# Kernel optimization log

Measured on AMD Instinct MI355X. Metric: run time of the kernel, lower is better.

## Reference

```python
import jax, jax.numpy as jnp
import numpy as np


def _sage_conv(x, src, dst, W_l, b_l, W_r, num_nodes):
    # PyG SAGEConv (aggr='mean'): out = lin_l(mean_j x[src_j]) + lin_r(x)
    msg = x[src]                                                  # [E, d]
    agg = jax.ops.segment_sum(msg, dst, num_segments=num_nodes)   # [N, d]
    deg = jax.ops.segment_sum(jnp.ones_like(dst, dtype=x.dtype), dst,
                              num_segments=num_nodes)             # [N]
    mean = agg / jnp.maximum(deg, 1.0)[:, None]
    return mean @ W_l + b_l + x @ W_r


def setup_inputs() -> dict:
    key = jax.random.key(0)
    ks = jax.random.split(key, 8)
    N, E, D = 50000, 640000, 128
    s = 1.0 / np.sqrt(D)
    return {
        "x": jax.random.normal(ks[0], (N, D), dtype=jnp.float32),
        "edge_index": jax.random.randint(ks[1], (2, E), 0, N, dtype=jnp.int64),
        "W1_l": jax.random.normal(ks[2], (D, D), dtype=jnp.float32) * s,
        "b1_l": jnp.zeros((D,), dtype=jnp.float32),
        "W1_r": jax.random.normal(ks[3], (D, D), dtype=jnp.float32) * s,
        "W2_l": jax.random.normal(ks[4], (D, D), dtype=jnp.float32) * s,
        "b2_l": jnp.zeros((D,), dtype=jnp.float32),
        "W2_r": jax.random.normal(ks[5], (D, D), dtype=jnp.float32) * s,
    }


def reference(x, edge_index, W1_l, b1_l, W1_r, W2_l, b2_l, W2_r):
    N = x.shape[0]
    src, dst = edge_index[0], edge_index[1]
    h = jax.nn.relu(_sage_conv(x, src, dst, W1_l, b1_l, W1_r, N))
    z = _sage_conv(h, src, dst, W2_l, b2_l, W2_r, N)
    return z
```

## Files before the change

### kernel.cpp

```cpp
#include <hip/hip_runtime.h>
#include <hip/hip_bf16.h>


#define CAP 64
#define NBLKA 128

#if __has_builtin(__builtin_amdgcn_global_load_lds)
#define HAS_GLDS 1
#endif

typedef __attribute__((ext_vector_type(8))) short short8v;
typedef __attribute__((ext_vector_type(4))) float float4v;

__device__ __forceinline__ ushort f2bf(float f) {
    unsigned u = __float_as_uint(f);
    u += 0x7fff + ((u >> 16) & 1);
    return (ushort)(u >> 16);
}

#if __has_builtin(__builtin_amdgcn_cvt_pk_fp8_f32) && __has_builtin(__builtin_amdgcn_cvt_f32_fp8)
#define HW_FP8 1
#endif

__device__ __forceinline__ float fp8_dec_sw(unsigned b) {
    unsigned s = b >> 7, e = (b >> 3) & 15, m = b & 7;
    float v = e ? __uint_as_float(((e + 120u) << 23) | (m << 20))
                : (float)m * 0.001953125f;
    return s ? -v : v;
}
__device__ __forceinline__ unsigned fp8_enc_sw(float f) {
    float aa = fabsf(f);
    unsigned e32 = __float_as_uint(aa) >> 23;
    float c = (aa < 0.015625f) ? 16384.f : __uint_as_float((e32 + 20) << 23);
    float r = (aa + c) - c;
    if (r > 448.f) r = 448.f;
    unsigned s = (__float_as_uint(f) >> 31) << 7;
    if (r == 0.f) return s;
    unsigned u = __float_as_uint(r);
    int e = (int)(u >> 23) - 127;
    if (e < -6) return s | (unsigned)(r * 512.f);
    return s | ((unsigned)(e + 7) << 3) | ((u >> 20) & 7);
}

__device__ __forceinline__ unsigned enc4_fp8(float4 v) {
#ifdef HW_FP8
    int p = 0;
    p = __builtin_amdgcn_cvt_pk_fp8_f32(v.x, v.y, p, false);
    p = __builtin_amdgcn_cvt_pk_fp8_f32(v.z, v.w, p, true);
    return (unsigned)p;
#else
    return fp8_enc_sw(v.x) | (fp8_enc_sw(v.y) << 8) |
           (fp8_enc_sw(v.z) << 16) | (fp8_enc_sw(v.w) << 24);
#endif
}
__device__ __forceinline__ unsigned char enc1_fp8(float v) {
#ifdef HW_FP8
    return (unsigned char)(__builtin_amdgcn_cvt_pk_fp8_f32(v, v, 0, false) & 0xff);
#else
    return (unsigned char)fp8_enc_sw(v);
#endif
}
template <int SEL>
__device__ __forceinline__ float dec_fp8(unsigned w) {
#ifdef HW_FP8
    return __builtin_amdgcn_cvt_f32_fp8(w, SEL);
#else
    return fp8_dec_sw((w >> (SEL * 8)) & 0xff);
#endif
}
__device__ __forceinline__ void acc4_fp8(float* a, unsigned w) {
    a[0] += dec_fp8<0>(w);
    a[1] += dec_fp8<1>(w);
    a[2] += dec_fp8<2>(w);
    a[3] += dec_fp8<3>(w);
}

__global__ __launch_bounds__(256) void prep_bin_kernel(
    const int* __restrict__ src, const int* __restrict__ dst, int E, int N, int nbuk,
    unsigned* __restrict__ seg, int* __restrict__ cntA,
    const float* __restrict__ X, ushort* __restrict__ Xb,
    unsigned* __restrict__ X8, int n4,
    const float* __restrict__ W1l, const float* __restrict__ W1r, ushort* __restrict__ Wt1,
    const float* __restrict__ W2l, const float* __restrict__ W2r, ushort* __restrict__ Wt2,
    int nConv) {
    int b = blockIdx.x;
    if (b < NBLKA) {
        __shared__ int cnt[512];
        for (int i = threadIdx.x; i < nbuk; i += 256) cnt[i] = 0;
        __syncthreads();
        const int EPB = ((E + NBLKA - 1) / NBLKA + 3) & ~3;
        const int e0 = b * EPB;
        const int e1 = min(E & ~3, e0 + EPB);
        const int4* d4p = reinterpret_cast<const int4*>(dst);
        const int4* s4p = reinterpret_cast<const int4*>(src);
        unsigned* myseg = seg + (size_t)b * nbuk * CAP;
        for (int e4 = (e0 >> 2) + threadIdx.x; e4 < (e1 >> 2); e4 += 256) {
            int4 d4 = d4p[e4];
            int4 s4 = s4p[e4];
#pragma unroll
            for (int j = 0; j < 4; ++j) {
                int d = (&d4.x)[j];
                int bu = d >> 8;
                int pos = atomicAdd(&cnt[bu], 1);
                if (pos < CAP)
                    myseg[bu * CAP + pos] =
                        ((unsigned)(d & 255) << 16) | (unsigned)((&s4.x)[j] & 0xffff);
            }
        }
        if (b == 0) {
            int t = threadIdx.x;
            if (t < (E & 3)) {
                int e = (E & ~3) + t;
                int d = dst[e];
                int bu = d >> 8;
                int pos = atomicAdd(&cnt[bu], 1);
                if (pos < CAP)
                    myseg[bu * CAP + pos] =
                        ((unsigned)(d & 255) << 16) | (unsigned)(src[e] & 0xffff);
            }
        }
        __syncthreads();
        for (int i = threadIdx.x; i < nbuk; i += 256)
            cntA[b * nbuk + i] = min(cnt[i], CAP);
    } else if (b < NBLKA + nConv) {
        int i = (b - NBLKA) * 256 + threadIdx.x;
        if (i < n4) {
            float4 v = reinterpret_cast<const float4*>(X)[i];
            ushort4 o;
            o.x = f2bf(v.x); o.y = f2bf(v.y); o.z = f2bf(v.z); o.w = f2bf(v.w);
            reinterpret_cast<ushort4*>(Xb)[i] = o;
            X8[i] = enc4_fp8(v);
        }
    } else {
        int wb = b - NBLKA - nConv;
        const float* Wl = (wb < 128) ? W1l : W2l;
        const float* Wr = (wb < 128) ? W1r : W2r;
        ushort* Wt = (wb < 128) ? Wt1 : Wt2;
        int col = wb & 127;
        int k = threadIdx.x;
        float v = (k < 128) ? Wl[k * 128 + col] : Wr[(k - 128) * 128 + col];
        int gr = k >> 3, sub = k & 7;
        Wt[(size_t)(col * 32 + (gr ^ (col & 7))) * 8 + sub] = f2bf(v);
    }
}

__global__ __launch_bounds__(256) void csr_build_kernel(
    const unsigned* __restrict__ seg, const int* __restrict__ cntA,
    ushort* __restrict__ csrc, int* __restrict__ cursor, int N, int nbuk) {
    __shared__ ushort lcs[256 * CAP];
    __shared__ int lcnt[256];
    __shared__ int scnt[NBLKA];
    const int b = blockIdx.x;
    const int tid = threadIdx.x;
    lcnt[tid] = 0;
    if (tid < NBLKA) scnt[tid] = cntA[tid * nbuk + b];
    __syncthreads();
    for (int idx = tid; idx < NBLKA * CAP; idx += 256) {
        int blk = idx >> 6, slot = idx & (CAP - 1);
        if (slot < scnt[blk]) {
            unsigned en = seg[((size_t)blk * nbuk + b) * CAP + slot];
            int local = (en >> 16) & 255;
            int pos = atomicAdd(&lcnt[local], 1);
            if (pos < CAP) lcs[local * CAP + pos] = (ushort)(en & 0xffff);
        }
    }
    __syncthreads();
    const int maxNode = min(256, N - b * 256);
    const uint4* s4 = reinterpret_cast<const uint4*>(lcs);
    uint4* d4 = reinterpret_cast<uint4*>(csrc + (size_t)b * 256 * CAP);
    for (int i = tid; i < maxNode * (CAP / 8); i += 256) d4[i] = s4[i];
    if (tid < maxNode) cursor[b * 256 + tid] = min(lcnt[tid], CAP);
}

__global__ __launch_bounds__(256) void gather_mean_fp8(
    const unsigned* __restrict__ X8, const int* __restrict__ cnt,
    const ushort* __restrict__ csrc, ushort* __restrict__ meanb, int N) {
    const int wid = __builtin_amdgcn_readfirstlane((blockIdx.x * 256 + threadIdx.x) >> 6);
    if (wid >= N) return;
    const int lane = threadIdx.x & 63;
    const int q = lane >> 4;
    const int lq = lane & 15;
    const int dc = min(cnt[wid], CAP);
    const ushort* ep = csrc + (size_t)wid * CAP;

    float acc[8];
#pragma unroll
    for (int j = 0; j < 8; ++j) acc[j] = 0.f;

    const uint2* Xp = reinterpret_cast<const uint2*>(X8);
    int e = 0;
#pragma unroll 4
    for (; e + 3 < dc; e += 4) {
        uint2 iw = *reinterpret_cast<const uint2*>(ep + e);
        unsigned wv = (q & 2) ? iw.y : iw.x;
        int s = (q & 1) ? (int)(wv >> 16) : (int)(wv & 0xffff);
        uint2 v = Xp[(size_t)s * 16 + lq];
        acc4_fp8(acc, v.x);
        acc4_fp8(acc + 4, v.y);
    }
    if (e + q < dc) {
        int s = ep[e + q];
        uint2 v = Xp[(size_t)s * 16 + lq];
        acc4_fp8(acc, v.x);
        acc4_fp8(acc + 4, v.y);
    }

#pragma unroll
    for (int j = 0; j < 8; ++j) {
        acc[j] += __shfl_xor(acc[j], 32);
        acc[j] += __shfl_xor(acc[j], 16);
    }

    if (q == 0) {
        float sc = 1.0f / (float)max(dc, 1);
        uint4 o;
        o.x = (unsigned)f2bf(acc[0] * sc) | ((unsigned)f2bf(acc[1] * sc) << 16);
        o.y = (unsigned)f2bf(acc[2] * sc) | ((unsigned)f2bf(acc[3] * sc) << 16);
        o.z = (unsigned)f2bf(acc[4] * sc) | ((unsigned)f2bf(acc[5] * sc) << 16);
        o.w = (unsigned)f2bf(acc[6] * sc) | ((unsigned)f2bf(acc[7] * sc) << 16);
        reinterpret_cast<uint4*>(meanb)[(size_t)wid * 16 + lq] = o;
    }
}

template <int RELU, int OUT_BF16, int WRITE_FP8>
__global__ __launch_bounds__(256) void sage_gemm_mfma(
    const ushort* __restrict__ A0,
    const ushort* __restrict__ A1,
    const ushort* __restrict__ Wt,
    const float* __restrict__ bias,
    void* __restrict__ outv,
    unsigned char* __restrict__ out8, int N) {
    __shared__ __align__(16) ushort Ws[128 * 256];
    const int tid = threadIdx.x;
    const int lane = tid & 63;
    const int wave = tid >> 6;
    const int r = lane & 15;
    const int g = lane >> 4;
    const int rt0 = blockIdx.x * 128 + wave * 32;

    int ar0 = rt0 + r;       if (ar0 >= N) ar0 = N - 1;
    int ar1 = rt0 + 16 + r;  if (ar1 >= N) ar1 = N - 1;

#ifdef HAS_GLDS
    {
        auto gp = (const __attribute__((address_space(1))) char*)(const char*)Wt;
        auto lp = (__attribute__((address_space(3))) char*)(char*)Ws;
#pragma unroll
        for (int it = 0; it < 16; ++it) {
            int G = it * 256 + tid;
            int Lw = (it * 256 + (tid & 192)) * 16;
            __builtin_amdgcn_global_load_lds(gp + (size_t)G * 16, lp + Lw, 16, 0, 0);
        }
    }
#else
    {
        const uint4* Wg = reinterpret_cast<const uint4*>(Wt);
        uint4* Ls = reinterpret_cast<uint4*>(Ws);
#pragma unroll
        for (int it = 0; it < 16; ++it) {
            int G = it * 256 + tid;
            Ls[G] = Wg[G];
        }
    }
#endif

    short8v af0[8], af1[8];
#pragma unroll
    for (int ks = 0; ks < 8; ++ks) {
        const ushort* Ap0 = ((ks < 4) ? A0 : A1) + (size_t)ar0 * 128;
        const ushort* Ap1 = ((ks < 4) ? A0 : A1) + (size_t)ar1 * 128;
        af0[ks] = *(const short8v*)(Ap0 + (ks & 3) * 32 + g * 8);
        af1[ks] = *(const short8v*)(Ap1 + (ks & 3) * 32 + g * 8);
    }

    float4v acc0[8], acc1[8];
#pragma unroll
    for (int ct = 0; ct < 8; ++ct) {
        float bv = bias[ct * 16 + r];
        acc0[ct] = (float4v){bv, bv, bv, bv};
        acc1[ct] = acc0[ct];
    }

    __syncthreads();

#pragma unroll
    for (int ks = 0; ks < 8; ++ks) {
#pragma unroll
        for (int ct = 0; ct < 8; ++ct) {
            const int col = ct * 16 + r;
            const int gr = (ks * 4 + g) ^ (r & 7);
            short8v bf = *(const short8v*)(Ws + col * 256 + gr * 8);
            acc0[ct] = __builtin_amdgcn_mfma_f32_16x16x32_bf16(af0[ks], bf, acc0[ct], 0, 0, 0);
            acc1[ct] = __builtin_amdgcn_mfma_f32_16x16x32_bf16(af1[ks], bf, acc1[ct], 0, 0, 0);
        }
    }

#pragma unroll
    for (int t = 0; t < 2; ++t) {
        const int rbase = rt0 + t * 16;
        float4v* acc = t ? acc1 : acc0;
#pragma unroll
        for (int ct = 0; ct < 8; ++ct) {
            const int col = ct * 16 + r;
#pragma unroll
            for (int reg = 0; reg < 4; ++reg) {
                int orow = rbase + g * 4 + reg;
                if (orow < N) {
                    float v = acc[ct][reg];
                    if (RELU) v = fmaxf(v, 0.f);
                    if (OUT_BF16)
                        ((ushort*)outv)[(size_t)orow * 128 + col] = f2bf(v);
                    else
                        ((float*)outv)[(size_t)orow * 128 + col] = v;
                    if (WRITE_FP8)
                        out8[(size_t)orow * 128 + col] = enc1_fp8(v);
                }
            }
        }
    }
}


extern "C" void kernel_launch(void* const* d_in, const int* in_sizes, int n_in,
                              void* d_out, int out_size, void* d_ws, size_t ws_size,
                              hipStream_t stream) {
    const float* x   = (const float*)d_in[0];
    const int*   ei  = (const int*)d_in[1];
    const float* W1l = (const float*)d_in[2];
    const float* b1  = (const float*)d_in[3];
    const float* W1r = (const float*)d_in[4];
    const float* W2l = (const float*)d_in[5];
    const float* b2  = (const float*)d_in[6];
    const float* W2r = (const float*)d_in[7];
    float* out = (float*)d_out;

    const int D = 128;
    const int N = in_sizes[0] / D;
    const int E = in_sizes[1] / 2;
    const int nbuk = (N + 255) >> 8;

    const int* srcp = ei;
    const int* dstp = ei + E;

    char* ws = (char*)d_ws;
    ushort*   xb     = (ushort*)ws;
    ushort*   hb     = xb + (size_t)N * D;
    ushort*   meanb  = hb + (size_t)N * D;
    ushort*   Wt1    = meanb + (size_t)N * D;
    ushort*   Wt2    = Wt1 + 128 * 256;
    unsigned* x8     = (unsigned*)(Wt2 + 128 * 256);
    unsigned* h8     = x8 + (size_t)N * D / 4;
    ushort*   csrc   = (ushort*)(h8 + (size_t)N * D / 4);
    int*      cursor = (int*)(csrc + (size_t)N * CAP);
    unsigned* seg    = (unsigned*)(cursor + ((N + 3) & ~3));
    int*      cntA   = (int*)(seg + (size_t)NBLKA * nbuk * CAP);

    const int n4 = N * D / 4;
    const int nConv = (n4 + 255) / 256;

    prep_bin_kernel<<<NBLKA + nConv + 256, 256, 0, stream>>>(
        srcp, dstp, E, N, nbuk, seg, cntA, x, xb, x8, n4,
        W1l, W1r, Wt1, W2l, W2r, Wt2, nConv);

    csr_build_kernel<<<nbuk, 256, 0, stream>>>(seg, cntA, csrc, cursor, N, nbuk);

    const int gather_blocks = (N * 64 + 255) / 256;
    const int gemm_blocks = (N + 127) / 128;

    gather_mean_fp8<<<gather_blocks, 256, 0, stream>>>(x8, cursor, csrc, meanb, N);
    sage_gemm_mfma<1, 1, 1><<<gemm_blocks, 256, 0, stream>>>(
        meanb, xb, Wt1, b1, hb, (unsigned char*)h8, N);

    gather_mean_fp8<<<gather_blocks, 256, 0, stream>>>(h8, cursor, csrc, meanb, N);
    sage_gemm_mfma<0, 0, 0><<<gemm_blocks, 256, 0, stream>>>(
        meanb, hb, Wt2, b2, out, nullptr, N);
}
```

Baseline: 100.5 us.

## Reorder layer-2 as transform-then-aggregate and fuse both GEMMs into one kernel

Uses linearity of the mean to compute h@W2_l (and h@W2_r+b2) right after layer 1 inside one fused kernel. The second gather then averages pre-projected fp8 rows and adds the self term, which removes the separate layer-2 GEMM launch and the h round-trip through global memory. It trades this for two layer-2 GEMMs per block, a reload of the weight tile into LDS, and smaller 64-row blocks. The projected messages are quantized to fp8 after the matmul rather than before it, which changes the error characteristics.

Result: faster. 97.79 us (-2.7%).

```diff
diff --git a/kernel.cpp b/kernel.cpp
--- a/kernel.cpp
+++ b/kernel.cpp
@@ -17,6 +17,8 @@
     u += 0x7fff + ((u >> 16) & 1);
     return (ushort)(u >> 16);
 }
+__device__ __forceinline__ float bflo(unsigned v) { return __uint_as_float(v << 16); }
+__device__ __forceinline__ float bfhi(unsigned v) { return __uint_as_float(v & 0xffff0000u); }
 
 #if __has_builtin(__builtin_amdgcn_cvt_pk_fp8_f32) && __has_builtin(__builtin_amdgcn_cvt_f32_fp8)
 #define HW_FP8 1
@@ -222,28 +224,30 @@
     }
 }
 
-template <int RELU, int OUT_BF16, int WRITE_FP8>
-__global__ __launch_bounds__(256) void sage_gemm_mfma(
+__global__ __launch_bounds__(256) void sage_layer1_fused(
     const ushort* __restrict__ A0,
     const ushort* __restrict__ A1,
-    const ushort* __restrict__ Wt,
-    const float* __restrict__ bias,
-    void* __restrict__ outv,
-    unsigned char* __restrict__ out8, int N) {
+    const ushort* __restrict__ Wt1,
+    const ushort* __restrict__ Wt2,
+    const float* __restrict__ b1, const float* __restrict__ b2,
+    unsigned char* __restrict__ p2_8,
+    ushort* __restrict__ s2,
+    int N) {
     __shared__ __align__(16) ushort Ws[128 * 256];
+    __shared__ __align__(16) ushort Hs[64 * 128];
     const int tid = threadIdx.x;
     const int lane = tid & 63;
     const int wave = tid >> 6;
     const int r = lane & 15;
     const int g = lane >> 4;
-    const int rt0 = blockIdx.x * 128 + wave * 32;
-
-    int ar0 = rt0 + r;       if (ar0 >= N) ar0 = N - 1;
-    int ar1 = rt0 + 16 + r;  if (ar1 >= N) ar1 = N - 1;
+    const int rt0 = blockIdx.x * 64 + wave * 16;
+
+    int ar = rt0 + r;
+    if (ar >= N) ar = N - 1;
 
 #ifdef HAS_GLDS
     {
-        auto gp = (const __attribute__((address_space(1))) char*)(const char*)Wt;
+        auto gp = (const __attribute__((address_space(1))) char*)(const char*)Wt1;
         auto lp = (__attribute__((address_space(3))) char*)(char*)Ws;
 #pragma unroll
         for (int it = 0; it < 16; ++it) {
@@ -254,31 +258,25 @@
     }
 #else
     {
-        const uint4* Wg = reinterpret_cast<const uint4*>(Wt);
+        const uint4* Wg = reinterpret_cast<const uint4*>(Wt1);
         uint4* Ls = reinterpret_cast<uint4*>(Ws);
 #pragma unroll
-        for (int it = 0; it < 16; ++it) {
-            int G = it * 256 + tid;
-            Ls[G] = Wg[G];
-        }
-    }
-#endif
-
-    short8v af0[8], af1[8];
+        for (int it = 0; it < 16; ++it) { int G = it * 256 + tid; Ls[G] = Wg[G]; }
+    }
+#endif
+
+    short8v af[8];
 #pragma unroll
     for (int ks = 0; ks < 8; ++ks) {
-        const ushort* Ap0 = ((ks < 4) ? A0 : A1) + (size_t)ar0 * 128;
-        const ushort* Ap1 = ((ks < 4) ? A0 : A1) + (size_t)ar1 * 128;
-        af0[ks] = *(const short8v*)(Ap0 + (ks & 3) * 32 + g * 8);
-        af1[ks] = *(const short8v*)(Ap1 + (ks & 3) * 32 + g * 8);
-    }
-
-    float4v acc0[8], acc1[8];
+        const ushort* Ap = ((ks < 4) ? A0 : A1) + (size_t)ar * 128;
+        af[ks] = *(const short8v*)(Ap + (ks & 3) * 32 + g * 8);
+    }
+
+    float4v acc[8];
 #pragma unroll
     for (int ct = 0; ct < 8; ++ct) {
-        float bv = bias[ct * 16 + r];
-        acc0[ct] = (float4v){bv, bv, bv, bv};
-        acc1[ct] = acc0[ct];
+        float bv = b1[ct * 16 + r];
+        acc[ct] = (float4v){bv, bv, bv, bv};
     }
 
     __syncthreads();
@@ -290,33 +288,146 @@
             const int col = ct * 16 + r;
             const int gr = (ks * 4 + g) ^ (r & 7);
             short8v bf = *(const short8v*)(Ws + col * 256 + gr * 8);
-            acc0[ct] = __builtin_amdgcn_mfma_f32_16x16x32_bf16(af0[ks], bf, acc0[ct], 0, 0, 0);
-            acc1[ct] = __builtin_amdgcn_mfma_f32_16x16x32_bf16(af1[ks], bf, acc1[ct], 0, 0, 0);
-        }
-    }
-
-#pragma unroll
-    for (int t = 0; t < 2; ++t) {
-        const int rbase = rt0 + t * 16;
-        float4v* acc = t ? acc1 : acc0;
+            acc[ct] = __builtin_amdgcn_mfma_f32_16x16x32_bf16(af[ks], bf, acc[ct], 0, 0, 0);
+        }
+    }
+
+    {
+        ushort* hw = Hs + wave * 16 * 128;
 #pragma unroll
         for (int ct = 0; ct < 8; ++ct) {
             const int col = ct * 16 + r;
+            const int g0 = col >> 3;
 #pragma unroll
             for (int reg = 0; reg < 4; ++reg) {
-                int orow = rbase + g * 4 + reg;
-                if (orow < N) {
-                    float v = acc[ct][reg];
-                    if (RELU) v = fmaxf(v, 0.f);
-                    if (OUT_BF16)
-                        ((ushort*)outv)[(size_t)orow * 128 + col] = f2bf(v);
-                    else
-                        ((float*)outv)[(size_t)orow * 128 + col] = v;
-                    if (WRITE_FP8)
-                        out8[(size_t)orow * 128 + col] = enc1_fp8(v);
-                }
+                const int row = g * 4 + reg;
+                float v = fmaxf(acc[ct][reg], 0.f);
+                hw[row * 128 + ((g0 ^ (row & 7)) * 8 + (col & 7))] = f2bf(v);
             }
         }
+    }
+
+    __syncthreads();
+
+#ifdef HAS_GLDS
+    {
+        auto gp = (const __attribute__((address_space(1))) char*)(const char*)Wt2;
+        auto lp = (__attribute__((address_space(3))) char*)(char*)Ws;
+#pragma unroll
+        for (int it = 0; it < 16; ++it) {
+            int G = it * 256 + tid;
+            int Lw = (it * 256 + (tid & 192)) * 16;
+            __builtin_amdgcn_global_load_lds(gp + (size_t)G * 16, lp + Lw, 16, 0, 0);
+        }
+    }
+#else
+    {
+        const uint4* Wg = reinterpret_cast<const uint4*>(Wt2);
+        uint4* Ls = reinterpret_cast<uint4*>(Ws);
+#pragma unroll
+        for (int it = 0; it < 16; ++it) { int G = it * 256 + tid; Ls[G] = Wg[G]; }
+    }
+#endif
+
+    short8v ah[4];
+    {
+        const ushort* hw = Hs + wave * 16 * 128;
+#pragma unroll
+        for (int ks = 0; ks < 4; ++ks) {
+            const int gr = (ks * 4 + g) ^ (r & 7);
+            ah[ks] = *(const short8v*)(hw + r * 128 + gr * 8);
+        }
+    }
+
+    float4v accp[8], accs[8];
+#pragma unroll
+    for (int ct = 0; ct < 8; ++ct) {
+        float bv = b2[ct * 16 + r];
+        accp[ct] = (float4v){0.f, 0.f, 0.f, 0.f};
+        accs[ct] = (float4v){bv, bv, bv, bv};
+    }
+
+    __syncthreads();
+
+#pragma unroll
+    for (int ks = 0; ks < 4; ++ks) {
+#pragma unroll
+        for (int ct = 0; ct < 8; ++ct) {
+            const int col = ct * 16 + r;
+            const int grp = (ks * 4 + g) ^ (r & 7);
+            const int grs = 16 + (((ks + 4 - 4) * 4 + g) ^ (r & 7));
+            short8v bp = *(const short8v*)(Ws + col * 256 + grp * 8);
+            short8v bs = *(const short8v*)(Ws + col * 256 + grs * 8);
+            accp[ct] = __builtin_amdgcn_mfma_f32_16x16x32_bf16(ah[ks], bp, accp[ct], 0, 0, 0);
+            accs[ct] = __builtin_amdgcn_mfma_f32_16x16x32_bf16(ah[ks], bs, accs[ct], 0, 0, 0);
+        }
+    }
+
+#pragma unroll
+    for (int ct = 0; ct < 8; ++ct) {
+        const int col = ct * 16 + r;
+#pragma unroll
+        for (int reg = 0; reg < 4; ++reg) {
+            int orow = rt0 + g * 4 + reg;
+            if (orow < N) {
+                p2_8[(size_t)orow * 128 + col] = enc1_fp8(accp[ct][reg]);
+                s2[(size_t)orow * 128 + col] = f2bf(accs[ct][reg]);
+            }
+        }
+    }
+}
+
+__global__ __launch_bounds__(256) void gather_final(
+    const unsigned* __restrict__ P8, const int* __restrict__ cnt,
+    const ushort* __restrict__ csrc, const ushort* __restrict__ s2,
+    float* __restrict__ out, int N) {
+    const int wid = __builtin_amdgcn_readfirstlane((blockIdx.x * 256 + threadIdx.x) >> 6);
+    if (wid >= N) return;
+    const int lane = threadIdx.x & 63;
+    const int q = lane >> 4;
+    const int lq = lane & 15;
+    const int dc = min(cnt[wid], CAP);
+    const ushort* ep = csrc + (size_t)wid * CAP;
+
+    float acc[8];
+#pragma unroll
+    for (int j = 0; j < 8; ++j) acc[j] = 0.f;
+
+    const uint2* Xp = reinterpret_cast<const uint2*>(P8);
+    int e = 0;
+#pragma unroll 4
+    for (; e + 3 < dc; e += 4) {
+        uint2 iw = *reinterpret_cast<const uint2*>(ep + e);
+        unsigned wv = (q & 2) ? iw.y : iw.x;
+        int s = (q & 1) ? (int)(wv >> 16) : (int)(wv & 0xffff);
+        uint2 v = Xp[(size_t)s * 16 + lq];
+        acc4_fp8(acc, v.x);
+        acc4_fp8(acc + 4, v.y);
+    }
+    if (e + q < dc) {
+        int s = ep[e + q];
+        uint2 v = Xp[(size_t)s * 16 + lq];
+        acc4_fp8(acc, v.x);
+        acc4_fp8(acc + 4, v.y);
+    }
+
+#pragma unroll
+    for (int j = 0; j < 8; ++j) {
+        acc[j] += __shfl_xor(acc[j], 32);
+        acc[j] += __shfl_xor(acc[j], 16);
+    }
+
+    if (q == 0) {
+        float sc = 1.0f / (float)max(dc, 1);
+        uint4 sv = reinterpret_cast<const uint4*>(s2)[(size_t)wid * 16 + lq];
+        float4 o0, o1;
+        o0.x = acc[0] * sc + bflo(sv.x); o0.y = acc[1] * sc + bfhi(sv.x);
+        o0.z = acc[2] * sc + bflo(sv.y); o0.w = acc[3] * sc + bfhi(sv.y);
+        o1.x = acc[4] * sc + bflo(sv.z); o1.y = acc[5] * sc + bfhi(sv.z);
+        o1.z = acc[6] * sc + bflo(sv.w); o1.w = acc[7] * sc + bfhi(sv.w);
+        float4* op = reinterpret_cast<float4*>(out + (size_t)wid * 128 + lq * 8);
+        op[0] = o0;
+        op[1] = o1;
     }
 }
 
@@ -344,13 +455,13 @@
 
     char* ws = (char*)d_ws;
     ushort*   xb     = (ushort*)ws;
-    ushort*   hb     = xb + (size_t)N * D;
-    ushort*   meanb  = hb + (size_t)N * D;
-    ushort*   Wt1    = meanb + (size_t)N * D;
+    ushort*   meanb  = xb + (size_t)N * D;
+    ushort*   s2     = meanb + (size_t)N * D;
+    ushort*   Wt1    = s2 + (size_t)N * D;
     ushort*   Wt2    = Wt1 + 128 * 256;
     unsigned* x8     = (unsigned*)(Wt2 + 128 * 256);
-    unsigned* h8     = x8 + (size_t)N * D / 4;
-    ushort*   csrc   = (ushort*)(h8 + (size_t)N * D / 4);
+    unsigned* p2_8   = x8 + (size_t)N * D / 4;
+    ushort*   csrc   = (ushort*)(p2_8 + (size_t)N * D / 4);
     int*      cursor = (int*)(csrc + (size_t)N * CAP);
     unsigned* seg    = (unsigned*)(cursor + ((N + 3) & ~3));
     int*      cntA   = (int*)(seg + (size_t)NBLKA * nbuk * CAP);
@@ -365,13 +476,11 @@
     csr_build_kernel<<<nbuk, 256, 0, stream>>>(seg, cntA, csrc, cursor, N, nbuk);
 
     const int gather_blocks = (N * 64 + 255) / 256;
-    const int gemm_blocks = (N + 127) / 128;
 
     gather_mean_fp8<<<gather_blocks, 256, 0, stream>>>(x8, cursor, csrc, meanb, N);
-    sage_gemm_mfma<1, 1, 1><<<gemm_blocks, 256, 0, stream>>>(
-        meanb, xb, Wt1, b1, hb, (unsigned char*)h8, N);
-
-    gather_mean_fp8<<<gather_blocks, 256, 0, stream>>>(h8, cursor, csrc, meanb, N);
-    sage_gemm_mfma<0, 0, 0><<<gemm_blocks, 256, 0, stream>>>(
-        meanb, hb, Wt2, b2, out, nullptr, N);
-}
+
+    sage_layer1_fused<<<(N + 63) / 64, 256, 0, stream>>>(
+        meanb, xb, Wt1, Wt2, b1, b2, (unsigned char*)p2_8, s2, N);
+
+    gather_final<<<gather_blocks, 256, 0, stream>>>(p2_8, cursor, csrc, s2, out, N);
+}
```
